# Kernel tuning notes

Measured on AMD Instinct MI355X. Metric: run time of the kernel, lower is better.

The kernel has to match this reference:

```python
import jax, jax.numpy as jnp
import numpy as np

# Configuration (mirrors BatchWiseSimCLR with batch_size=64, mask_size=512, temperature=0.5)
B = 64          # args.batch_size
TWO_B = 2 * B   # 128
K = 256         # number of chunks of size 2B in x (and in x_pair); K + K = mask_size
MS = 512        # mask_size = K + K'
D = 256         # projection feature dim
TEMP = 0.5      # temperature
EPS = 1e-8      # torch F.cosine_similarity eps


def setup_inputs() -> dict:
    key = jax.random.key(0)
    k1, k2 = jax.random.split(key)
    x = jax.random.normal(k1, (TWO_B * K, D), dtype=jnp.float32)
    x_pair = jax.random.normal(k2, (TWO_B * K, D), dtype=jnp.float32)
    return {"x": x, "x_pair": x_pair}


def _cosine_sim(a, b):
    # torch.F.cosine_similarity: clamp each norm at eps
    na = jnp.maximum(jnp.linalg.norm(a, axis=-1), EPS)
    nb = jnp.maximum(jnp.linalg.norm(b, axis=-1), EPS)
    return jnp.sum(a * b, axis=-1) / (na * nb)


def reference(x, x_pair):
    # ---- positive loss ----
    # x.split(x_pair.shape[0]) yields a single chunk here (N == M), matching
    # the torch loop which keeps only the last chunk's loss.
    n_positives = x.shape[0] / x_pair.shape[0]  # == 1.0
    loss_pos = jnp.mean(_cosine_sim(x, x_pair) / TEMP / n_positives)

    # ---- negative loss ----
    # torch: cat of chunks of size 2B along new dim 1 -> element [r, i, :] = x[i*2B + r]
    x_r = x.reshape(K, TWO_B, D).transpose(1, 0, 2)        # [2B, K, D]
    xp_r = x_pair.reshape(K, TWO_B, D).transpose(1, 0, 2)  # [2B, K, D]
    z = jnp.concatenate([x_r, xp_r], axis=1)               # [2B, MS, D]

    zn = z / jnp.maximum(jnp.linalg.norm(z, axis=-1, keepdims=True), EPS)
    sim = jnp.einsum('bid,bjd->bij', zn, zn) / TEMP        # [2B, MS, MS]

    # mask diagonal (self-similarity) per batch element, logsumexp over the
    # remaining MS-1 entries of each row
    eye = jnp.eye(MS, dtype=bool)
    masked = jnp.where(eye[None, :, :], -jnp.inf, sim)
    loss_neg = jnp.mean(jax.scipy.special.logsumexp(masked, axis=2))

    return loss_neg - loss_pos
```

## Files before the change

### kernel.cpp

```cpp
#include <hip/hip_runtime.h>


#define TWO_B   128
#define MS      512
#define DDIM    256
#define NROWS   32768
#define TEMP_INV 2.0f
#define EPSN     1e-8f
#define SQRT2   1.41421356237f

typedef __attribute__((ext_vector_type(8))) short  short8;
typedef __attribute__((ext_vector_type(4))) float  f32x4;

__device__ __forceinline__ unsigned short f2bf(float f) {
  union { float f; unsigned u; } c; c.f = f;
  unsigned r = (c.u + 0x7FFFu + ((c.u >> 16) & 1u)) >> 16;
  return (unsigned short)r;
}

#define GLDS16(gp, lp)                                                         \
  __builtin_amdgcn_global_load_lds(                                            \
      (const __attribute__((address_space(1))) unsigned int*)(gp),             \
      (__attribute__((address_space(3))) unsigned int*)(lp), 16, 0, 0)


__global__ __launch_bounds__(256) void k_norm_f(
    const float* __restrict__ x, const float* __restrict__ xp,
    unsigned short* __restrict__ zn) {
  const int wid = threadIdx.x >> 6, lane = threadIdx.x & 63;
  #pragma unroll
  for (int itr = 0; itr < 4; ++itr) {
    const int r = itr * 8192 + blockIdx.x * 4 + wid;
    const int b = r & 127, i = r >> 7;
    const float4 a = ((const float4*)(x  + (size_t)r * DDIM))[lane];
    const float4 p = ((const float4*)(xp + (size_t)r * DDIM))[lane];
    float sxx = a.x*a.x + a.y*a.y + a.z*a.z + a.w*a.w;
    float spp = p.x*p.x + p.y*p.y + p.z*p.z + p.w*p.w;
    #pragma unroll
    for (int m = 1; m < 64; m <<= 1) {
      sxx += __shfl_xor(sxx, m);
      spp += __shfl_xor(spp, m);
    }
    const float inx = SQRT2 / fmaxf(sqrtf(sxx), EPSN);
    const float inp = SQRT2 / fmaxf(sqrtf(spp), EPSN);
    const int us = (lane * 4) ^ ((i & 7) << 3);
    ushort4 ox, op;
    ox.x = f2bf(a.x * inx); ox.y = f2bf(a.y * inx);
    ox.z = f2bf(a.z * inx); ox.w = f2bf(a.w * inx);
    op.x = f2bf(p.x * inp); op.y = f2bf(p.y * inp);
    op.z = f2bf(p.z * inp); op.w = f2bf(p.w * inp);
    *(ushort4*)(zn + ((size_t)(b * MS + i)       * DDIM) + us) = ox;
    *(ushort4*)(zn + ((size_t)(b * MS + 256 + i) * DDIM) + us) = op;
  }
}

__device__ __forceinline__ void stage_b(const unsigned short* g,
                                        unsigned short* d, int wid, int lane) {
  #pragma unroll
  for (int s = 0; s < 8; ++s) {
    const int c = wid * 8 + s;
    GLDS16(g + c * 512 + lane * 8, d + c * 512);
  }
}

__global__ __launch_bounds__(256) void k_neg_f(
    const unsigned short* __restrict__ zn,
    float* __restrict__ negp, float* __restrict__ posn) {
  __shared__ __align__(16) unsigned short buf[2][64 * 256];
  const int b  = blockIdx.x;
  const int it = blockIdx.y;
  const int lane = threadIdx.x & 63, wid = threadIdx.x >> 6;

  {
    const unsigned short* gA = zn + (size_t)(b * MS + it * 128) * DDIM;
    #pragma unroll
    for (int s = 0; s < 8; ++s) {
      const int c = wid * 8 + s;
      GLDS16(gA + c * 512 + lane * 8, buf[0] + c * 512);
      GLDS16(gA + 32768 + c * 512 + lane * 8, buf[1] + c * 512);
    }
  }
  __syncthreads();

  short8 av[2][8];
  {
    const unsigned short* src = buf[wid >> 1];
    #pragma unroll
    for (int rb = 0; rb < 2; ++rb) {
      const int ar = (wid & 1) * 32 + rb * 16 + (lane & 15);
      #pragma unroll
      for (int kk = 0; kk < 8; ++kk) {
        const int col = kk * 32 + ((lane >> 4) << 3);
        av[rb][kk] = *(const short8*)(src + ar * 256 + (col ^ ((ar & 7) << 3)));
      }
    }
  }
  __syncthreads();

  const unsigned short* gB = zn + (size_t)b * MS * DDIM;
  stage_b(gB, buf[0], wid, lane);
  stage_b(gB + 32768, buf[1], wid, lane);

  float rowacc[2][4] = {{0,0,0,0},{0,0,0,0}};
  float posl = 0.0f;

  #pragma unroll
  for (int jt = 0; jt < 8; ++jt) {
    if (jt == 7) asm volatile("s_waitcnt vmcnt(0)" ::: "memory");
    else         asm volatile("s_waitcnt vmcnt(8)" ::: "memory");
    __builtin_amdgcn_sched_barrier(0);
    __builtin_amdgcn_s_barrier();
    __builtin_amdgcn_sched_barrier(0);

    const unsigned short* Bsrc = buf[jt & 1];
    f32x4 acc[2][4] = {{{0,0,0,0},{0,0,0,0},{0,0,0,0},{0,0,0,0}},
                       {{0,0,0,0},{0,0,0,0},{0,0,0,0},{0,0,0,0}}};
    #pragma unroll
    for (int kk = 0; kk < 8; ++kk) {
      const int col = kk * 32 + ((lane >> 4) << 3);
      #pragma unroll
      for (int ni = 0; ni < 4; ++ni) {
        const int br = ni * 16 + (lane & 15);
        const short8 bv = *(const short8*)(Bsrc + br * 256 + (col ^ ((br & 7) << 3)));
        acc[0][ni] = __builtin_amdgcn_mfma_f32_16x16x32_bf16(av[0][kk], bv, acc[0][ni], 0, 0, 0);
        acc[1][ni] = __builtin_amdgcn_mfma_f32_16x16x32_bf16(av[1][kk], bv, acc[1][ni], 0, 0, 0);
      }
    }

    #pragma unroll
    for (int rb = 0; rb < 2; ++rb) {
      const int igb = it * 128 + wid * 32 + rb * 16 + ((lane >> 4) << 2);
      #pragma unroll
      for (int ni = 0; ni < 4; ++ni) {
        const int jg = jt * 64 + ni * 16 + (lane & 15);
        #pragma unroll
        for (int r2 = 0; r2 < 4; ++r2) {
          const int ig = igb + r2;
          const float s = acc[rb][ni][r2];
          rowacc[rb][r2] += (ig == jg) ? 0.0f : __expf(s);
          posl += (ig + 256 == jg) ? s : 0.0f;
        }
      }
    }
    __builtin_amdgcn_sched_barrier(0);
    __builtin_amdgcn_s_barrier();
    __builtin_amdgcn_sched_barrier(0);
    if (jt < 6) stage_b(gB + (size_t)(jt + 2) * 32768, buf[jt & 1], wid, lane);
  }

  float partial = 0.0f;
  #pragma unroll
  for (int rb = 0; rb < 2; ++rb)
    #pragma unroll
    for (int r2 = 0; r2 < 4; ++r2) {
      float v = rowacc[rb][r2];
      v += __shfl_xor(v, 1); v += __shfl_xor(v, 2);
      v += __shfl_xor(v, 4); v += __shfl_xor(v, 8);
      partial += __logf(v);
    }
  partial += __shfl_xor(partial, 16);
  partial += __shfl_xor(partial, 32);
  #pragma unroll
  for (int m = 1; m < 64; m <<= 1) posl += __shfl_xor(posl, m);

  __shared__ float sn[4], sp2[4];
  if (lane == 0) { sn[wid] = partial; sp2[wid] = posl; }
  __syncthreads();
  if (threadIdx.x == 0) {
    const int bid = blockIdx.y * TWO_B + blockIdx.x;
    negp[bid] = sn[0] + sn[1] + sn[2] + sn[3];
    posn[bid] = sp2[0] + sp2[1] + sp2[2] + sp2[3];
  }
}

__global__ __launch_bounds__(256) void k_fin_f(
    const float* __restrict__ posn, const float* __restrict__ negp,
    float* __restrict__ out) {
  const int t = threadIdx.x, wid = t >> 6, lane = t & 63;
  float p = posn[t] + posn[t + 256];
  float n = negp[t] + negp[t + 256];
  #pragma unroll
  for (int m = 1; m < 64; m <<= 1) { p += __shfl_xor(p, m); n += __shfl_xor(n, m); }
  __shared__ float sp[4], sq[4];
  if (lane == 0) { sp[wid] = p; sq[wid] = n; }
  __syncthreads();
  if (t == 0) {
    const float pt = sp[0] + sp[1] + sp[2] + sp[3];
    const float nt = sq[0] + sq[1] + sq[2] + sq[3];
    out[0] = nt * (1.0f / 65536.0f) - pt * (1.0f / 32768.0f);
  }
}


__global__ __launch_bounds__(256) void k_norm(
    const float* __restrict__ x, const float* __restrict__ xp,
    float* __restrict__ invx, float* __restrict__ invp, float* __restrict__ posp) {
  const int wid = threadIdx.x >> 6, lane = threadIdx.x & 63;
  float posl = 0.0f;
  #pragma unroll
  for (int itr = 0; itr < 8; ++itr) {
    const int r = itr * 4096 + blockIdx.x * 4 + wid;
    const float4 a = ((const float4*)(x  + (size_t)r * DDIM))[lane];
    const float4 b = ((const float4*)(xp + (size_t)r * DDIM))[lane];
    float sxx = a.x*a.x + a.y*a.y + a.z*a.z + a.w*a.w;
    float spp = b.x*b.x + b.y*b.y + b.z*b.z + b.w*b.w;
    float sxp = a.x*b.x + a.y*b.y + a.z*b.z + a.w*b.w;
    #pragma unroll
    for (int m = 1; m < 64; m <<= 1) {
      sxx += __shfl_xor(sxx, m);
      spp += __shfl_xor(spp, m);
      sxp += __shfl_xor(sxp, m);
    }
    const float inx = 1.0f / fmaxf(sqrtf(sxx), EPSN);
    const float inp = 1.0f / fmaxf(sqrtf(spp), EPSN);
    if (lane == 0) {
      invx[r] = inx; invp[r] = inp;
      posl += sxp * inx * inp * TEMP_INV;
    }
  }
  __shared__ float cp[4];
  if (lane == 0) cp[wid] = posl;
  __syncthreads();
  if (threadIdx.x == 0) posp[blockIdx.x] = cp[0] + cp[1] + cp[2] + cp[3];
}

__device__ __forceinline__ void stage_tile(
    unsigned short* dst, const float* __restrict__ x, const float* __restrict__ xp,
    const float* __restrict__ invx, const float* __restrict__ invp, int b, int tilebase) {
  const int t = threadIdx.x;
  const bool isp = (tilebase >= 256);
  const float* src = isp ? xp : x;
  const float* inv = isp ? invp : invx;
  const int base_i = isp ? (tilebase - 256) : tilebase;
  #pragma unroll
  for (int s = 0; s < 16; ++s) {
    const int u   = s * 256 + t;
    const int row = u >> 6, c4 = u & 63;
    const int g   = (base_i + row) * TWO_B + b;
    const float4 v = *(const float4*)(src + (size_t)g * DDIM + c4 * 4);
    const float sc = inv[g];
    ushort4 o;
    o.x = f2bf(v.x * sc); o.y = f2bf(v.y * sc);
    o.z = f2bf(v.z * sc); o.w = f2bf(v.w * sc);
    *(ushort4*)(dst + row * 256 + ((c4 * 4) ^ ((row & 7) << 3))) = o;
  }
}

__global__ __launch_bounds__(256, 2) void k_neg(
    const float* __restrict__ x, const float* __restrict__ xp,
    const float* __restrict__ invx, const float* __restrict__ invp,
    float* __restrict__ negp) {
  __shared__ __align__(16) unsigned short As[64 * 256];
  __shared__ __align__(16) unsigned short Bs[64 * 256];
  const int b  = blockIdx.x;
  const int it = blockIdx.y;
  const int lane = threadIdx.x & 63, wid = threadIdx.x >> 6;

  stage_tile(As, x, xp, invx, invp, b, it * 64);
  float rowacc[4] = {0, 0, 0, 0};

  for (int jt = 0; jt < 8; ++jt) {
    __syncthreads();
    stage_tile(Bs, x, xp, invx, invp, b, jt * 64);
    __syncthreads();

    f32x4 acc[4] = {{0,0,0,0},{0,0,0,0},{0,0,0,0},{0,0,0,0}};
    #pragma unroll
    for (int kk = 0; kk < 8; ++kk) {
      const int col = kk * 32 + ((lane >> 4) << 3);
      const int ar  = wid * 16 + (lane & 15);
      const short8 av = *(const short8*)(As + ar * 256 + (col ^ ((ar & 7) << 3)));
      #pragma unroll
      for (int ni = 0; ni < 4; ++ni) {
        const int br = ni * 16 + (lane & 15);
        const short8 bv = *(const short8*)(Bs + br * 256 + (col ^ ((br & 7) << 3)));
        acc[ni] = __builtin_amdgcn_mfma_f32_16x16x32_bf16(av, bv, acc[ni], 0, 0, 0);
      }
    }
    const int igb = it * 64 + wid * 16 + ((lane >> 4) << 2);
    #pragma unroll
    for (int ni = 0; ni < 4; ++ni) {
      const int jg = jt * 64 + ni * 16 + (lane & 15);
      #pragma unroll
      for (int r2 = 0; r2 < 4; ++r2) {
        const float s = acc[ni][r2] * TEMP_INV;
        rowacc[r2] += ((igb + r2) == jg) ? 0.0f : __expf(s);
      }
    }
  }

  float partial = 0.0f;
  #pragma unroll
  for (int r2 = 0; r2 < 4; ++r2) {
    float v = rowacc[r2];
    v += __shfl_xor(v, 1); v += __shfl_xor(v, 2);
    v += __shfl_xor(v, 4); v += __shfl_xor(v, 8);
    partial += __logf(v);
  }
  partial += __shfl_xor(partial, 16);
  partial += __shfl_xor(partial, 32);

  __shared__ float sn[4];
  if (lane == 0) sn[wid] = partial;
  __syncthreads();
  if (threadIdx.x == 0)
    negp[blockIdx.y * TWO_B + blockIdx.x] = sn[0] + sn[1] + sn[2] + sn[3];
}

__global__ __launch_bounds__(256) void k_fin(
    const float* __restrict__ posp, const float* __restrict__ negp,
    float* __restrict__ out) {
  const int t = threadIdx.x, wid = t >> 6, lane = t & 63;
  const float4 p4 = ((const float4*)posp)[t];
  const float4 n4 = ((const float4*)negp)[t];
  float p = p4.x + p4.y + p4.z + p4.w;
  float n = n4.x + n4.y + n4.z + n4.w;
  #pragma unroll
  for (int m = 1; m < 64; m <<= 1) { p += __shfl_xor(p, m); n += __shfl_xor(n, m); }
  __shared__ float sp[4], sq[4];
  if (lane == 0) { sp[wid] = p; sq[wid] = n; }
  __syncthreads();
  if (t == 0) {
    const float pt = sp[0] + sp[1] + sp[2] + sp[3];
    const float nt = sq[0] + sq[1] + sq[2] + sq[3];
    out[0] = nt * (1.0f / 65536.0f) - pt * (1.0f / 32768.0f);
  }
}

extern "C" void kernel_launch(void* const* d_in, const int* in_sizes, int n_in,
                              void* d_out, int out_size, void* d_ws, size_t ws_size,
                              hipStream_t stream) {
  const float* x  = (const float*)d_in[0];
  const float* xp = (const float*)d_in[1];
  float* wsf = (float*)d_ws;
  float* out = (float*)d_out;

  const size_t need_fast = 4096 + (size_t)65536 * DDIM * 2;
  if (ws_size >= need_fast) {
    float* negp = wsf;
    float* posn = wsf + 512;
    unsigned short* zn = (unsigned short*)(wsf + 1024);
    k_norm_f<<<2048, 256, 0, stream>>>(x, xp, zn);
    k_neg_f<<<dim3(TWO_B, 4), 256, 0, stream>>>(zn, negp, posn);
    k_fin_f<<<1, 256, 0, stream>>>(posn, negp, out);
  } else {
    float* invx = wsf;
    float* invp = wsf + NROWS;
    float* posp = wsf + 2 * NROWS;
    float* negp = wsf + 2 * NROWS + 1024;
    k_norm<<<1024, 256, 0, stream>>>(x, xp, invx, invp, posp);
    k_neg<<<dim3(TWO_B, 8), 256, 0, stream>>>(x, xp, invx, invp, negp);
    k_fin<<<1, 256, 0, stream>>>(posp, negp, out);
  }
}
```

Baseline: 121.3 us.

## Software-pipeline exp epilogue of previous tile with MFMA of current tile

Double-buffers the accumulator registers so that the exp/logsumexp epilogue for tile jt-1 is issued alongside the MFMA loop for tile jt, letting VALU transcendental work overlap matrix-core work. The MFMA section is wrapped in s_setprio to favor issuing matrix instructions. The diagonal and positive masks are also simplified to tile-level compile-time checks plus a lane compare. This doubles accumulator register use, which may raise VGPR pressure and reduce occupancy.

```diff
diff --git a/kernel.cpp b/kernel.cpp
--- a/kernel.cpp
+++ b/kernel.cpp
@@ -103,6 +103,33 @@
 
   float rowacc[2][4] = {{0,0,0,0},{0,0,0,0}};
   float posl = 0.0f;
+  f32x4 acc[2][2][4];
+
+  const int ri = (lane >> 4) << 2;
+  const int ci = lane & 15;
+  const int tb0 = it * 128 + wid * 32;
+
+  #define EPILOGUE(t)                                                          \
+    {                                                                          \
+      _Pragma("unroll")                                                        \
+      for (int rb = 0; rb < 2; ++rb) {                                         \
+        const int tb = tb0 + rb * 16;                                          \
+        _Pragma("unroll")                                                      \
+        for (int ni = 0; ni < 4; ++ni) {                                       \
+          const int jtb = (t) * 64 + ni * 16;                                  \
+          const bool dtile = (jtb == tb);                    \
+          const bool ptile = (jtb == tb + 256);              \
+          _Pragma("unroll")                                                    \
+          for (int r2 = 0; r2 < 4; ++r2) {                                     \
+            const float s = acc[(t) & 1][rb][ni][r2];                          \
+            float e = __expf(s);                                               \
+            if (dtile && ci == ri + r2) e = 0.0f;                              \
+            rowacc[rb][r2] += e;                                               \
+            if (ptile && ci == ri + r2) posl += s;                             \
+          }                                                                    \
+        }                                                                      \
+      }                                                                        \
+    }
 
   #pragma unroll
   for (int jt = 0; jt < 8; ++jt) {
@@ -113,8 +140,15 @@
     __builtin_amdgcn_sched_barrier(0);
 
     const unsigned short* Bsrc = buf[jt & 1];
-    f32x4 acc[2][4] = {{{0,0,0,0},{0,0,0,0},{0,0,0,0},{0,0,0,0}},
-                       {{0,0,0,0},{0,0,0,0},{0,0,0,0},{0,0,0,0}}};
+    #pragma unroll
+    for (int rb = 0; rb < 2; ++rb)
+      #pragma unroll
+      for (int ni = 0; ni < 4; ++ni)
+        acc[jt & 1][rb][ni] = (f32x4){0, 0, 0, 0};
+
+    if (jt >= 1) EPILOGUE(jt - 1);
+
+    __builtin_amdgcn_s_setprio(1);
     #pragma unroll
     for (int kk = 0; kk < 8; ++kk) {
       const int col = kk * 32 + ((lane >> 4) << 3);
@@ -122,31 +156,19 @@
       for (int ni = 0; ni < 4; ++ni) {
         const int br = ni * 16 + (lane & 15);
         const short8 bv = *(const short8*)(Bsrc + br * 256 + (col ^ ((br & 7) << 3)));
-        acc[0][ni] = __builtin_amdgcn_mfma_f32_16x16x32_bf16(av[0][kk], bv, acc[0][ni], 0, 0, 0);
-        acc[1][ni] = __builtin_amdgcn_mfma_f32_16x16x32_bf16(av[1][kk], bv, acc[1][ni], 0, 0, 0);
+        acc[jt & 1][0][ni] = __builtin_amdgcn_mfma_f32_16x16x32_bf16(av[0][kk], bv, acc[jt & 1][0][ni], 0, 0, 0);
+        acc[jt & 1][1][ni] = __builtin_amdgcn_mfma_f32_16x16x32_bf16(av[1][kk], bv, acc[jt & 1][1][ni], 0, 0, 0);
       }
     }
-
-    #pragma unroll
-    for (int rb = 0; rb < 2; ++rb) {
-      const int igb = it * 128 + wid * 32 + rb * 16 + ((lane >> 4) << 2);
-      #pragma unroll
-      for (int ni = 0; ni < 4; ++ni) {
-        const int jg = jt * 64 + ni * 16 + (lane & 15);
-        #pragma unroll
-        for (int r2 = 0; r2 < 4; ++r2) {
-          const int ig = igb + r2;
-          const float s = acc[rb][ni][r2];
-          rowacc[rb][r2] += (ig == jg) ? 0.0f : __expf(s);
-          posl += (ig + 256 == jg) ? s : 0.0f;
-        }
-      }
-    }
+    __builtin_amdgcn_s_setprio(0);
+
     __builtin_amdgcn_sched_barrier(0);
     __builtin_amdgcn_s_barrier();
     __builtin_amdgcn_sched_barrier(0);
     if (jt < 6) stage_b(gB + (size_t)(jt + 2) * 32768, buf[jt & 1], wid, lane);
   }
+  EPILOGUE(7);
+  #undef EPILOGUE
 
   float partial = 0.0f;
   #pragma unroll
```

New measurement: 119.1 us. About the same (-1.9%).

## Retile negative-loss GEMM to 256x256 tiles with split column halves

Applied to the files above, without the earlier changes.

The negative-similarity kernel now gives each block 256 rows and half of the columns, so each wave holds 64 rows of A in registers read straight from global memory. Per-row exp sums for each column half are written to a workspace, and the log is taken in a larger 1024-thread final kernel. MFMA sections raise wave priority, and the next B tile is staged before the exp epilogue so loads overlap compute. The goal is more MFMA reuse per LDS B read and better overlap. The cost is higher register pressure, a larger workspace, and a heavier single-block final reduction.

```diff
diff --git a/kernel.cpp b/kernel.cpp
--- a/kernel.cpp
+++ b/kernel.cpp
@@ -63,130 +63,140 @@
   }
 }
 
-__global__ __launch_bounds__(256) void k_neg_f(
+__global__ __launch_bounds__(256, 2) void k_neg_f2(
     const unsigned short* __restrict__ zn,
-    float* __restrict__ negp, float* __restrict__ posn) {
-  __shared__ __align__(16) unsigned short buf[2][64 * 256];
+    float* __restrict__ rowsumh, float* __restrict__ posn) {
+  __shared__ __align__(16) unsigned short sh[2][64 * 256];
   const int b  = blockIdx.x;
   const int it = blockIdx.y;
+  const int jh = blockIdx.z;
   const int lane = threadIdx.x & 63, wid = threadIdx.x >> 6;
-
-  {
-    const unsigned short* gA = zn + (size_t)(b * MS + it * 128) * DDIM;
-    #pragma unroll
-    for (int s = 0; s < 8; ++s) {
-      const int c = wid * 8 + s;
-      GLDS16(gA + c * 512 + lane * 8, buf[0] + c * 512);
-      GLDS16(gA + 32768 + c * 512 + lane * 8, buf[1] + c * 512);
-    }
-  }
-  __syncthreads();
-
-  short8 av[2][8];
-  {
-    const unsigned short* src = buf[wid >> 1];
-    #pragma unroll
-    for (int rb = 0; rb < 2; ++rb) {
-      const int ar = (wid & 1) * 32 + rb * 16 + (lane & 15);
-      #pragma unroll
-      for (int kk = 0; kk < 8; ++kk) {
-        const int col = kk * 32 + ((lane >> 4) << 3);
-        av[rb][kk] = *(const short8*)(src + ar * 256 + (col ^ ((ar & 7) << 3)));
-      }
-    }
-  }
-  __syncthreads();
-
-  const unsigned short* gB = zn + (size_t)b * MS * DDIM;
-  stage_b(gB, buf[0], wid, lane);
-  stage_b(gB + 32768, buf[1], wid, lane);
-
-  float rowacc[2][4] = {{0,0,0,0},{0,0,0,0}};
+  const int l15 = lane & 15, hi = lane >> 4;
+  const int ri = hi << 2;
+
+  short8 av[4][8];
+  #pragma unroll
+  for (int rb = 0; rb < 4; ++rb) {
+    const int arow = it * 256 + wid * 64 + rb * 16 + l15;
+    const unsigned short* gr = zn + (size_t)(b * MS + arow) * DDIM;
+    const int swz = (arow & 7) << 3;
+    #pragma unroll
+    for (int kk = 0; kk < 8; ++kk) {
+      const int col = kk * 32 + (hi << 3);
+      av[rb][kk] = *(const short8*)(gr + (col ^ swz));
+    }
+  }
+
+  const unsigned short* gB = zn + (size_t)(b * MS + jh * 256) * DDIM;
+  stage_b(gB, sh[0], wid, lane);
+  stage_b(gB + 32768, sh[1], wid, lane);
+  __syncthreads();
+
+  float rowacc[4][4] = {{0,0,0,0},{0,0,0,0},{0,0,0,0},{0,0,0,0}};
   float posl = 0.0f;
 
   #pragma unroll
-  for (int jt = 0; jt < 8; ++jt) {
-    if (jt == 7) asm volatile("s_waitcnt vmcnt(0)" ::: "memory");
+  for (int jt = 0; jt < 4; ++jt) {
+    if (jt == 3) asm volatile("s_waitcnt vmcnt(0)" ::: "memory");
     else         asm volatile("s_waitcnt vmcnt(8)" ::: "memory");
     __builtin_amdgcn_sched_barrier(0);
     __builtin_amdgcn_s_barrier();
     __builtin_amdgcn_sched_barrier(0);
 
-    const unsigned short* Bsrc = buf[jt & 1];
-    f32x4 acc[2][4] = {{{0,0,0,0},{0,0,0,0},{0,0,0,0},{0,0,0,0}},
-                       {{0,0,0,0},{0,0,0,0},{0,0,0,0},{0,0,0,0}}};
+    const unsigned short* Bsrc = sh[jt & 1];
+    f32x4 acc[4][4];
+    #pragma unroll
+    for (int rb = 0; rb < 4; ++rb)
+      #pragma unroll
+      for (int ni = 0; ni < 4; ++ni)
+        acc[rb][ni] = (f32x4){0, 0, 0, 0};
+
+    __builtin_amdgcn_s_setprio(1);
     #pragma unroll
     for (int kk = 0; kk < 8; ++kk) {
-      const int col = kk * 32 + ((lane >> 4) << 3);
+      const int col = kk * 32 + (hi << 3);
       #pragma unroll
       for (int ni = 0; ni < 4; ++ni) {
-        const int br = ni * 16 + (lane & 15);
+        const int br = ni * 16 + l15;
         const short8 bv = *(const short8*)(Bsrc + br * 256 + (col ^ ((br & 7) << 3)));
-        acc[0][ni] = __builtin_amdgcn_mfma_f32_16x16x32_bf16(av[0][kk], bv, acc[0][ni], 0, 0, 0);
-        acc[1][ni] = __builtin_amdgcn_mfma_f32_16x16x32_bf16(av[1][kk], bv, acc[1][ni], 0, 0, 0);
-      }
-    }
-
-    #pragma unroll
-    for (int rb = 0; rb < 2; ++rb) {
-      const int igb = it * 128 + wid * 32 + rb * 16 + ((lane >> 4) << 2);
-      #pragma unroll
-      for (int ni = 0; ni < 4; ++ni) {
-        const int jg = jt * 64 + ni * 16 + (lane & 15);
         #pragma unroll
-        for (int r2 = 0; r2 < 4; ++r2) {
-          const int ig = igb + r2;
-          const float s = acc[rb][ni][r2];
-          rowacc[rb][r2] += (ig == jg) ? 0.0f : __expf(s);
-          posl += (ig + 256 == jg) ? s : 0.0f;
-        }
-      }
-    }
+        for (int rb = 0; rb < 4; ++rb)
+          acc[rb][ni] = __builtin_amdgcn_mfma_f32_16x16x32_bf16(av[rb][kk], bv, acc[rb][ni], 0, 0, 0);
+      }
+    }
+    __builtin_amdgcn_s_setprio(0);
+
     __builtin_amdgcn_sched_barrier(0);
     __builtin_amdgcn_s_barrier();
     __builtin_amdgcn_sched_barrier(0);
-    if (jt < 6) stage_b(gB + (size_t)(jt + 2) * 32768, buf[jt & 1], wid, lane);
-  }
-
-  float partial = 0.0f;
-  #pragma unroll
-  for (int rb = 0; rb < 2; ++rb)
+    if (jt < 2) stage_b(gB + (size_t)(jt + 2) * 32768, sh[jt & 1], wid, lane);
+
+    #pragma unroll
+    for (int rb = 0; rb < 4; ++rb) {
+      const int tb = it * 256 + wid * 64 + rb * 16;
+      #pragma unroll
+      for (int ni = 0; ni < 4; ++ni) {
+        const int jtb = jh * 256 + jt * 64 + ni * 16;
+        const bool dtile = (jtb == tb);
+        const bool ptile = (jtb == tb + 256);
+        #pragma unroll
+        for (int r2 = 0; r2 < 4; ++r2) {
+          const float s = acc[rb][ni][r2];
+          float e = __expf(s);
+          if (dtile && l15 == ri + r2) e = 0.0f;
+          rowacc[rb][r2] += e;
+          if (ptile && l15 == ri + r2) posl += s;
+        }
+      }
+    }
+  }
+
+  #pragma unroll
+  for (int rb = 0; rb < 4; ++rb)
     #pragma unroll
     for (int r2 = 0; r2 < 4; ++r2) {
       float v = rowacc[rb][r2];
       v += __shfl_xor(v, 1); v += __shfl_xor(v, 2);
       v += __shfl_xor(v, 4); v += __shfl_xor(v, 8);
-      partial += __logf(v);
-    }
-  partial += __shfl_xor(partial, 16);
-  partial += __shfl_xor(partial, 32);
+      if (l15 == rb * 4 + r2) {
+        const int row = it * 256 + wid * 64 + rb * 16 + ri + r2;
+        rowsumh[((size_t)jh * TWO_B + b) * MS + row] = v;
+      }
+    }
+
   #pragma unroll
   for (int m = 1; m < 64; m <<= 1) posl += __shfl_xor(posl, m);
-
-  __shared__ float sn[4], sp2[4];
-  if (lane == 0) { sn[wid] = partial; sp2[wid] = posl; }
-  __syncthreads();
-  if (threadIdx.x == 0) {
-    const int bid = blockIdx.y * TWO_B + blockIdx.x;
-    negp[bid] = sn[0] + sn[1] + sn[2] + sn[3];
-    posn[bid] = sp2[0] + sp2[1] + sp2[2] + sp2[3];
-  }
-}
-
-__global__ __launch_bounds__(256) void k_fin_f(
-    const float* __restrict__ posn, const float* __restrict__ negp,
+  __shared__ float sp2[4];
+  if (lane == 0) sp2[wid] = posl;
+  __syncthreads();
+  if (threadIdx.x == 0)
+    posn[(blockIdx.z * 2 + blockIdx.y) * TWO_B + blockIdx.x] =
+        sp2[0] + sp2[1] + sp2[2] + sp2[3];
+}
+
+__global__ __launch_bounds__(1024) void k_fin_f2(
+    const float* __restrict__ rowsumh, const float* __restrict__ posn,
     float* __restrict__ out) {
   const int t = threadIdx.x, wid = t >> 6, lane = t & 63;
-  float p = posn[t] + posn[t + 256];
-  float n = negp[t] + negp[t + 256];
-  #pragma unroll
-  for (int m = 1; m < 64; m <<= 1) { p += __shfl_xor(p, m); n += __shfl_xor(n, m); }
-  __shared__ float sp[4], sq[4];
-  if (lane == 0) { sp[wid] = p; sq[wid] = n; }
+  float nacc = 0.0f;
+  #pragma unroll 8
+  for (int i = 0; i < 64; ++i) {
+    const int r = i * 1024 + t;
+    nacc += __logf(rowsumh[r] + rowsumh[65536 + r]);
+  }
+  float pacc = (t < 512) ? posn[t] : 0.0f;
+  #pragma unroll
+  for (int m = 1; m < 64; m <<= 1) {
+    nacc += __shfl_xor(nacc, m);
+    pacc += __shfl_xor(pacc, m);
+  }
+  __shared__ float sn[16], sp[16];
+  if (lane == 0) { sn[wid] = nacc; sp[wid] = pacc; }
   __syncthreads();
   if (t == 0) {
-    const float pt = sp[0] + sp[1] + sp[2] + sp[3];
-    const float nt = sq[0] + sq[1] + sq[2] + sq[3];
+    float nt = 0.0f, pt = 0.0f;
+    #pragma unroll
+    for (int i = 0; i < 16; ++i) { nt += sn[i]; pt += sp[i]; }
     out[0] = nt * (1.0f / 65536.0f) - pt * (1.0f / 32768.0f);
   }
 }
@@ -335,14 +345,14 @@
   float* wsf = (float*)d_ws;
   float* out = (float*)d_out;
 
-  const size_t need_fast = 4096 + (size_t)65536 * DDIM * 2;
+  const size_t need_fast = (size_t)131584 * 4 + (size_t)65536 * DDIM * 2;
   if (ws_size >= need_fast) {
-    float* negp = wsf;
-    float* posn = wsf + 512;
-    unsigned short* zn = (unsigned short*)(wsf + 1024);
+    float* rowsumh = wsf;
+    float* posn = wsf + 131072;
+    unsigned short* zn = (unsigned short*)(wsf + 131584);
     k_norm_f<<<2048, 256, 0, stream>>>(x, xp, zn);
-    k_neg_f<<<dim3(TWO_B, 4), 256, 0, stream>>>(zn, negp, posn);
-    k_fin_f<<<1, 256, 0, stream>>>(posn, negp, out);
+    k_neg_f2<<<dim3(TWO_B, 2, 2), 256, 0, stream>>>(zn, rowsumh, posn);
+    k_fin_f2<<<1, 1024, 0, stream>>>(rowsumh, posn, out);
   } else {
     float* invx = wsf;
     float* invp = wsf + NROWS;
```

Measured after the change: 149.3 us. +23.0%, slower.

## Triple-buffer smaller B tiles and overlap exp epilogue with next prefetch

Applied to the files above, without the earlier changes.

The negative-similarity kernel now stages B in 32-row tiles across three LDS buffers instead of 64-row tiles in two, which cuts shared memory and allows three blocks per CU via launch bounds. A operands load directly from global memory instead of passing through LDS. The next tile's prefetch is issued before the exp/logsumexp epilogue so the load overlaps the math, and the MFMA loop runs at raised wave priority. The mask checks are simplified to per-tile tests, at the cost of more barrier iterations with fewer MFMAs each.

```diff
diff --git a/kernel.cpp b/kernel.cpp
--- a/kernel.cpp
+++ b/kernel.cpp
@@ -54,98 +54,97 @@
   }
 }
 
-__device__ __forceinline__ void stage_b(const unsigned short* g,
-                                        unsigned short* d, int wid, int lane) {
-  #pragma unroll
-  for (int s = 0; s < 8; ++s) {
-    const int c = wid * 8 + s;
+__device__ __forceinline__ void stage_b32(const unsigned short* g,
+                                          unsigned short* d, int wid, int lane) {
+  #pragma unroll
+  for (int s = 0; s < 4; ++s) {
+    const int c = wid * 4 + s;
     GLDS16(g + c * 512 + lane * 8, d + c * 512);
   }
 }
 
-__global__ __launch_bounds__(256) void k_neg_f(
+__global__ __launch_bounds__(256, 3) void k_neg_f4(
     const unsigned short* __restrict__ zn,
     float* __restrict__ negp, float* __restrict__ posn) {
-  __shared__ __align__(16) unsigned short buf[2][64 * 256];
+  __shared__ __align__(16) unsigned short sh[3][32 * 256];
   const int b  = blockIdx.x;
   const int it = blockIdx.y;
   const int lane = threadIdx.x & 63, wid = threadIdx.x >> 6;
-
-  {
-    const unsigned short* gA = zn + (size_t)(b * MS + it * 128) * DDIM;
-    #pragma unroll
-    for (int s = 0; s < 8; ++s) {
-      const int c = wid * 8 + s;
-      GLDS16(gA + c * 512 + lane * 8, buf[0] + c * 512);
-      GLDS16(gA + 32768 + c * 512 + lane * 8, buf[1] + c * 512);
-    }
-  }
-  __syncthreads();
+  const int l15 = lane & 15, hi = lane >> 4;
+  const int ri = hi << 2;
 
   short8 av[2][8];
-  {
-    const unsigned short* src = buf[wid >> 1];
-    #pragma unroll
-    for (int rb = 0; rb < 2; ++rb) {
-      const int ar = (wid & 1) * 32 + rb * 16 + (lane & 15);
-      #pragma unroll
-      for (int kk = 0; kk < 8; ++kk) {
-        const int col = kk * 32 + ((lane >> 4) << 3);
-        av[rb][kk] = *(const short8*)(src + ar * 256 + (col ^ ((ar & 7) << 3)));
-      }
-    }
-  }
-  __syncthreads();
+  #pragma unroll
+  for (int rb = 0; rb < 2; ++rb) {
+    const int arow = it * 128 + wid * 32 + rb * 16 + l15;
+    const unsigned short* gr = zn + (size_t)(b * MS + arow) * DDIM;
+    const int swz = (arow & 7) << 3;
+    #pragma unroll
+    for (int kk = 0; kk < 8; ++kk) {
+      const int col = kk * 32 + (hi << 3);
+      av[rb][kk] = *(const short8*)(gr + (col ^ swz));
+    }
+  }
 
   const unsigned short* gB = zn + (size_t)b * MS * DDIM;
-  stage_b(gB, buf[0], wid, lane);
-  stage_b(gB + 32768, buf[1], wid, lane);
+  stage_b32(gB,         sh[0], wid, lane);
+  stage_b32(gB + 8192,  sh[1], wid, lane);
+  stage_b32(gB + 16384, sh[2], wid, lane);
 
   float rowacc[2][4] = {{0,0,0,0},{0,0,0,0}};
   float posl = 0.0f;
 
   #pragma unroll
-  for (int jt = 0; jt < 8; ++jt) {
-    if (jt == 7) asm volatile("s_waitcnt vmcnt(0)" ::: "memory");
-    else         asm volatile("s_waitcnt vmcnt(8)" ::: "memory");
+  for (int jt = 0; jt < 16; ++jt) {
+    if (jt <= 13)      asm volatile("s_waitcnt vmcnt(8)" ::: "memory");
+    else if (jt == 14) asm volatile("s_waitcnt vmcnt(4)" ::: "memory");
+    else               asm volatile("s_waitcnt vmcnt(0)" ::: "memory");
     __builtin_amdgcn_sched_barrier(0);
     __builtin_amdgcn_s_barrier();
     __builtin_amdgcn_sched_barrier(0);
 
-    const unsigned short* Bsrc = buf[jt & 1];
-    f32x4 acc[2][4] = {{{0,0,0,0},{0,0,0,0},{0,0,0,0},{0,0,0,0}},
-                       {{0,0,0,0},{0,0,0,0},{0,0,0,0},{0,0,0,0}}};
+    const unsigned short* Bsrc = sh[jt % 3];
+    f32x4 acc[2][2];
+    acc[0][0] = (f32x4){0,0,0,0}; acc[0][1] = (f32x4){0,0,0,0};
+    acc[1][0] = (f32x4){0,0,0,0}; acc[1][1] = (f32x4){0,0,0,0};
+
+    __builtin_amdgcn_s_setprio(1);
     #pragma unroll
     for (int kk = 0; kk < 8; ++kk) {
-      const int col = kk * 32 + ((lane >> 4) << 3);
+      const int col = kk * 32 + (hi << 3);
       #pragma unroll
-      for (int ni = 0; ni < 4; ++ni) {
-        const int br = ni * 16 + (lane & 15);
+      for (int ni = 0; ni < 2; ++ni) {
+        const int br = ni * 16 + l15;
         const short8 bv = *(const short8*)(Bsrc + br * 256 + (col ^ ((br & 7) << 3)));
         acc[0][ni] = __builtin_amdgcn_mfma_f32_16x16x32_bf16(av[0][kk], bv, acc[0][ni], 0, 0, 0);
         acc[1][ni] = __builtin_amdgcn_mfma_f32_16x16x32_bf16(av[1][kk], bv, acc[1][ni], 0, 0, 0);
       }
     }
-
-    #pragma unroll
-    for (int rb = 0; rb < 2; ++rb) {
-      const int igb = it * 128 + wid * 32 + rb * 16 + ((lane >> 4) << 2);
-      #pragma unroll
-      for (int ni = 0; ni < 4; ++ni) {
-        const int jg = jt * 64 + ni * 16 + (lane & 15);
-        #pragma unroll
-        for (int r2 = 0; r2 < 4; ++r2) {
-          const int ig = igb + r2;
-          const float s = acc[rb][ni][r2];
-          rowacc[rb][r2] += (ig == jg) ? 0.0f : __expf(s);
-          posl += (ig + 256 == jg) ? s : 0.0f;
-        }
-      }
-    }
+    __builtin_amdgcn_s_setprio(0);
+
     __builtin_amdgcn_sched_barrier(0);
     __builtin_amdgcn_s_barrier();
     __builtin_amdgcn_sched_barrier(0);
-    if (jt < 6) stage_b(gB + (size_t)(jt + 2) * 32768, buf[jt & 1], wid, lane);
+    if (jt < 13) stage_b32(gB + (size_t)(jt + 3) * 8192, sh[jt % 3], wid, lane);
+
+    #pragma unroll
+    for (int rb = 0; rb < 2; ++rb) {
+      const int tb = it * 128 + wid * 32 + rb * 16;
+      #pragma unroll
+      for (int ni = 0; ni < 2; ++ni) {
+        const int jtb = jt * 32 + ni * 16;
+        const bool dtile = (jtb == tb);
+        const bool ptile = (jtb == tb + 256);
+        #pragma unroll
+        for (int r2 = 0; r2 < 4; ++r2) {
+          const float s = acc[rb][ni][r2];
+          float e = __expf(s);
+          if (dtile && l15 == ri + r2) e = 0.0f;
+          rowacc[rb][r2] += e;
+          if (ptile && l15 == ri + r2) posl += s;
+        }
+      }
+    }
   }
 
   float partial = 0.0f;
@@ -341,7 +340,7 @@
     float* posn = wsf + 512;
     unsigned short* zn = (unsigned short*)(wsf + 1024);
     k_norm_f<<<2048, 256, 0, stream>>>(x, xp, zn);
-    k_neg_f<<<dim3(TWO_B, 4), 256, 0, stream>>>(zn, negp, posn);
+    k_neg_f4<<<dim3(TWO_B, 4), 256, 0, stream>>>(zn, negp, posn);
     k_fin_f<<<1, 256, 0, stream>>>(posn, negp, out);
   } else {
     float* invx = wsf;
```

Result: no change. 120.5 us (-0.7%).
